# Kernel tuning notes

Measured on AMD Instinct MI355X. Metric: run time of the kernel, lower is better.

The kernel has to match this reference:

```python
import jax, jax.numpy as jnp
import numpy as np
from jax import lax

B, C, H, W = 16, 128, 64, 64
S = 16  # d_state


def setup_inputs() -> dict:
    key = jax.random.key(0)
    ks = jax.random.split(key, 12)
    d = {
        'x': jax.random.normal(ks[0], (B, C, H, W), jnp.float32),
        'conv_w': jax.random.normal(ks[1], (C, C, 3, 3), jnp.float32) * (1.0 / np.sqrt(C * 9)),
        'conv_b': jax.random.normal(ks[2], (C,), jnp.float32) * 0.01,
        'dt_w': jax.random.normal(ks[3], (C, C), jnp.float32) * (1.0 / np.sqrt(C)),
        'dt_b': jax.random.normal(ks[4], (C,), jnp.float32) * 0.01,
        'A': jax.random.normal(ks[5], (C, S), jnp.float32),
        'D': jax.random.normal(ks[6], (C,), jnp.float32),
        'g1_w': jax.random.normal(ks[7], (C, C), jnp.float32) * (1.0 / np.sqrt(C)),
        'g1_b': jax.random.normal(ks[8], (C,), jnp.float32) * 0.01,
        'g2_w': jax.random.normal(ks[9], (C, C), jnp.float32) * (1.0 / np.sqrt(C)),
        'g2_b': jax.random.normal(ks[10], (C,), jnp.float32) * 0.01,
    }
    return d


def _forward(x, conv_w, conv_b, dt_w, dt_b, A, D, g1_w, g1_b, g2_w, g2_b):
    identity = x
    # 3x3 conv, padding=1 (SAME)
    x = lax.conv_general_dilated(x, conv_w, (1, 1), 'SAME',
                                 dimension_numbers=('NCHW', 'OIHW', 'NCHW'))
    x = x + conv_b[None, :, None, None]
    # spectral gate: global avg pool -> 1x1 conv -> relu -> 1x1 conv -> sigmoid
    pooled = jnp.mean(x, axis=(2, 3))                       # [B, C]
    g = jax.nn.relu(jnp.einsum('bc,oc->bo', pooled, g1_w) + g1_b)
    g = jax.nn.sigmoid(jnp.einsum('bc,oc->bo', g, g2_w) + g2_b)
    x = x * g[:, :, None, None]
    # ssm scan over H*W tokens
    x_seq = x.transpose(0, 2, 3, 1).reshape(x.shape[0], H * W, C)  # [B, L, C]
    dt = jax.nn.sigmoid(jnp.einsum('blc,oc->blo', x_seq, dt_w) + dt_b)
    An = -jnp.exp(A)   # [C, S]
    Dp = jnp.exp(D)    # [C]

    def step(h, inp):
        xt, dtt = inp  # each [B, C]
        h = h * jnp.exp(An[None] * dtt[:, :, None]) + xt[:, :, None]  # [B, C, S]
        y = jnp.sum(h * An[None], axis=-1) + Dp * xt                   # [B, C]
        return h, y

    h0 = jnp.zeros((x.shape[0], C, S), x.dtype)
    xs = (x_seq.transpose(1, 0, 2), dt.transpose(1, 0, 2))  # [L, B, C]
    _, ys = lax.scan(step, h0, xs)                           # ys: [L, B, C]
    y = ys.transpose(1, 0, 2).reshape(x.shape[0], H, W, C).transpose(0, 3, 1, 2)
    return y + identity


def reference(x, conv_w, conv_b, dt_w, dt_b, A, D, g1_w, g1_b, g2_w, g2_b):
    return _forward(x, conv_w, conv_b, dt_w, dt_b, A, D, g1_w, g1_b, g2_w, g2_b)
```

## Files before the change

### kernel.cpp

```cpp
#include <hip/hip_runtime.h>
#include <hip/hip_bf16.h>
#include <stdint.h>

#define BB 16
#define CC 128
#define HH 64
#define WW 64
#define LL 4096
#define SS 16
#define NCH 64
#define CT 64

typedef __attribute__((ext_vector_type(2))) float f32x2;
typedef __attribute__((ext_vector_type(4))) float f32x4;
typedef __attribute__((ext_vector_type(8))) short short8;
typedef __attribute__((ext_vector_type(4))) unsigned int u32x4;

#define AS1 __attribute__((address_space(1)))
#define AS3 __attribute__((address_space(3)))

__device__ __forceinline__ float bf2f(unsigned short u) {
    union { unsigned int i; float f; } v;
    v.i = ((unsigned int)u) << 16;
    return v.f;
}
__device__ __forceinline__ float asf(unsigned int u) {
    union { unsigned int i; float f; } v;
    v.i = u;
    return v.f;
}
__device__ __forceinline__ unsigned short f2bf(float f) {
    union { float f; unsigned int i; } v;
    v.f = f;
    unsigned int x = v.i;
    return (unsigned short)((x + 0x7fffu + ((x >> 16) & 1u)) >> 16);
}
__device__ __forceinline__ float fexp2(float x) { return __builtin_amdgcn_exp2f(x); }

__global__ __launch_bounds__(256) void k0(const float* __restrict__ x, unsigned short* __restrict__ xT,
                                          const float* __restrict__ conv_w, const float* __restrict__ dt_w,
                                          const float* __restrict__ A, const float* __restrict__ Dv,
                                          const float* __restrict__ g1w, const float* __restrict__ g2w,
                                          short* __restrict__ wf, short* __restrict__ wdtf,
                                          float* __restrict__ An, float* __restrict__ An2, float* __restrict__ Dp,
                                          float* __restrict__ pooled, float* __restrict__ g1wT, float* __restrict__ g2wT) {
    __shared__ float lt[64][65];
    int bid = blockIdx.x;
    int tid = threadIdx.x;
    if (bid < 2048) {
        int b = bid >> 7, rem = bid & 127;
        int tt = rem >> 1, ct = rem & 1;
        int t0 = tt * 64, c0 = ct * 64;
        int colr = tid & 63, rowb = tid >> 6;
#pragma unroll
        for (int r = 0; r < 16; ++r) {
            int row = rowb + r * 4;
            lt[row][colr] = x[(size_t)(b * CC + c0 + row) * LL + t0 + colr];
        }
        __syncthreads();
#pragma unroll
        for (int r = 0; r < 16; ++r) {
            int trow = rowb + r * 4;
            xT[((size_t)b * LL + t0 + trow) * CC + c0 + colr] = f2bf(lt[colr][trow]);
        }
        return;
    }
    int idx = (bid - 2048) * 256 + tid;
    if (idx < 18432) {
        int lane = idx & 63, fr = idx >> 6;
        int nfg = fr & 7, ks = (fr >> 3) & 3, tp = fr >> 5;
        int dy = tp / 3, dx = tp % 3;
        int cout = nfg * 16 + (lane & 15);
        int cin0 = ks * 32 + (lane >> 4) * 8;
        short8 v;
#pragma unroll
        for (int j = 0; j < 8; ++j)
            v[j] = (short)f2bf(conv_w[((cout * CC + cin0 + j) * 3 + dy) * 3 + dx]);
        *(short8*)(wf + (size_t)idx * 8) = v;
    } else if (idx < 20480) {
        int i2 = idx - 18432;
        int lane = i2 & 63, fr = i2 >> 6;
        int nfg = fr & 7, ks = fr >> 3;
        int o = nfg * 16 + (lane & 15);
        int c0 = ks * 32 + (lane >> 4) * 8;
        short8 v;
#pragma unroll
        for (int j = 0; j < 8; ++j) v[j] = (short)f2bf(dt_w[o * CC + c0 + j]);
        *(short8*)(wdtf + (size_t)i2 * 8) = v;
    } else if (idx < 22528) {
        int i3 = idx - 20480;
        float a = -expf(A[i3]);
        An[i3] = a;
        An2[i3] = a * 1.4426950408889634f;
    } else if (idx < 22656) {
        int c = idx - 22528;
        Dp[c] = expf(Dv[c]);
    } else if (idx < 24704) {
        pooled[idx - 22656] = 0.f;
    } else if (idx < 41088) {
        int i = idx - 24704;
        int c = i >> 7, o = i & 127;
        g1wT[i] = g1w[o * 128 + c];
    } else if (idx < 57472) {
        int i = idx - 41088;
        int c = i >> 7, o = i & 127;
        g2wT[i] = g2w[o * 128 + c];
    }
}

__global__ __launch_bounds__(256) void k1(const unsigned short* __restrict__ xT,
                                          const short* __restrict__ wf,
                                          const float* __restrict__ conv_b,
                                          unsigned short* __restrict__ convT,
                                          float* __restrict__ pooled) {
    __shared__ __align__(16) unsigned short slab[3 * 66 * 128];
    int bid = blockIdx.x;
    int b = bid >> 6, h = bid & 63;
    int tid = threadIdx.x;
    int wave = tid >> 6, lane = tid & 63;

    if (tid < 96) {
        int dy = tid >> 5, r = (tid >> 4) & 1, j = tid & 15;
        u32x4 z = {0, 0, 0, 0};
        *(u32x4*)((char*)slab + dy * 16896 + (r ? 16640 : 0) + j * 16) = z;
    }
#pragma unroll
    for (int dy = 0; dy < 3; ++dy) {
        int hs = h + dy - 1;
        char* slabdy = (char*)slab + dy * 16896;
        if (hs >= 0 && hs < HH) {
            const char* src = (const char*)xT + (size_t)(b * LL + hs * 64) * 256;
#pragma unroll
            for (int i = 0; i < 4; ++i) {
                unsigned int Xbase = 256u + (unsigned)i * 4096u + (unsigned)wave * 1024u;
                unsigned int X = Xbase + (unsigned)lane * 16u;
                unsigned int tok = X >> 8;
                unsigned int srcoff = ((X & ~255u) - 256u) | ((X & 255u) ^ ((tok & 7u) << 4));
                __builtin_amdgcn_global_load_lds((const AS1 unsigned int*)(src + srcoff),
                                                 (AS3 unsigned int*)(slabdy + Xbase), 16, 0, 0);
            }
        } else {
            u32x4 z = {0, 0, 0, 0};
#pragma unroll
            for (int i = 0; i < 4; ++i)
                *(u32x4*)(slabdy + 256 + tid * 64 + i * 16) = z;
        }
    }
    __syncthreads();

    int lm = lane & 15, lg = lane >> 4;
    f32x4 acc[4][2];
#pragma unroll
    for (int m = 0; m < 4; ++m)
#pragma unroll
        for (int n = 0; n < 2; ++n) acc[m][n] = (f32x4){0.f, 0.f, 0.f, 0.f};

#pragma unroll
    for (int tp = 0; tp < 9; ++tp) {
        int dy = tp / 3, dx = tp % 3;
        const char* slabdy = (const char*)slab + dy * 16896;
#pragma unroll
        for (int ks = 0; ks < 4; ++ks) {
            short8 bf0 = *(const short8*)(wf + ((size_t)(((tp * 4 + ks) * 8) + wave * 2 + 0) * 64 + lane) * 8);
            short8 bf1 = *(const short8*)(wf + ((size_t)(((tp * 4 + ks) * 8) + wave * 2 + 1) * 64 + lane) * 8);
#pragma unroll
            for (int mf = 0; mf < 4; ++mf) {
                int tok = mf * 16 + lm + dx;
                unsigned int off = (unsigned)((tok * 256 + ks * 64 + lg * 16) ^ ((tok & 7) << 4));
                short8 af = *(const short8*)(slabdy + off);
                acc[mf][0] = __builtin_amdgcn_mfma_f32_16x16x32_bf16(af, bf0, acc[mf][0], 0, 0, 0);
                acc[mf][1] = __builtin_amdgcn_mfma_f32_16x16x32_bf16(af, bf1, acc[mf][1], 0, 0, 0);
            }
        }
    }

    int n0w = wave * 32;
    size_t tokbase = (size_t)(b * LL + h * 64);
    float psum[2] = {0.f, 0.f};
#pragma unroll
    for (int nf = 0; nf < 2; ++nf) {
        int n = n0w + nf * 16 + lm;
        float bias = conv_b[n];
#pragma unroll
        for (int mf = 0; mf < 4; ++mf)
#pragma unroll
            for (int r = 0; r < 4; ++r) {
                int w = mf * 16 + lg * 4 + r;
                float v = acc[mf][nf][r] + bias;
                convT[(tokbase + w) * CC + n] = f2bf(v);
                psum[nf] += v;
            }
    }
#pragma unroll
    for (int nf = 0; nf < 2; ++nf) {
        float s = psum[nf];
        s += __shfl_xor(s, 16);
        s += __shfl_xor(s, 32);
        if (lane < 16) atomicAdd(&pooled[b * CC + n0w + nf * 16 + lane], s);
    }
}

__global__ __launch_bounds__(128) void k2(const float* __restrict__ pooled,
                                          const float* __restrict__ g1wT, const float* __restrict__ g1b,
                                          const float* __restrict__ g2wT, const float* __restrict__ g2b,
                                          float* __restrict__ gate) {
    __shared__ float meanr[128];
    __shared__ float garr[128];
    int b = blockIdx.x;
    int tid = threadIdx.x;
    meanr[tid] = pooled[b * CC + tid] * (1.f / 4096.f);
    __syncthreads();
    float acc = g1b[tid];
    for (int c = 0; c < 128; ++c) acc += meanr[c] * g1wT[c * 128 + tid];
    garr[tid] = fmaxf(acc, 0.f);
    __syncthreads();
    float acc2 = g2b[tid];
    for (int c = 0; c < 128; ++c) acc2 += garr[c] * g2wT[c * 128 + tid];
    gate[b * CC + tid] = __builtin_amdgcn_rcpf(1.f + fexp2(-1.4426950408889634f * acc2));
}

__global__ __launch_bounds__(256) void k3(const unsigned short* __restrict__ convT,
                                          const short* __restrict__ wdtf,
                                          const float* __restrict__ gate,
                                          const float* __restrict__ dt_b,
                                          const float* __restrict__ An2,
                                          unsigned short* __restrict__ dtT,
                                          unsigned int* __restrict__ xdt,
                                          float* __restrict__ hend, float* __restrict__ decay,
                                          int packed) {
    __shared__ __align__(16) unsigned short albuf[64 * 128];
    __shared__ __align__(16) unsigned short dtl[64 * 136];
    __shared__ float gl[128];
    int bid = blockIdx.x;
    int b = bid >> 6, ch = bid & 63, t0 = ch * 64;
    int tid = threadIdx.x;
    int wave = tid >> 6, lane = tid & 63;

    if (tid < 128) gl[tid] = gate[b * CC + tid];
    __syncthreads();

    const char* srcb = (const char*)convT + (size_t)(b * LL + t0) * 256;
#pragma unroll
    for (int i = 0; i < 4; ++i) {
        unsigned int byteoff = (unsigned)((i * 256 + tid) * 16);
        unsigned int tok = byteoff >> 8;
        unsigned int inner = byteoff & 255u;
        int c8 = (int)(inner >> 1);
        short8 v = *(const short8*)(srcb + (size_t)tok * 256 + inner);
#pragma unroll
        for (int j = 0; j < 8; ++j) {
            float f = bf2f((unsigned short)v[j]) * gl[c8 + j];
            v[j] = (short)f2bf(f);
        }
        *(short8*)((char*)albuf + (byteoff ^ ((tok & 7u) << 4))) = v;
    }
    __syncthreads();

    int lm = lane & 15, lg = lane >> 4;
    f32x4 acc[4][2];
#pragma unroll
    for (int m = 0; m < 4; ++m)
#pragma unroll
        for (int n = 0; n < 2; ++n) acc[m][n] = (f32x4){0.f, 0.f, 0.f, 0.f};
#pragma unroll
    for (int ks = 0; ks < 4; ++ks) {
        short8 bf0 = *(const short8*)(wdtf + ((size_t)((ks * 8) + wave * 2 + 0) * 64 + lane) * 8);
        short8 bf1 = *(const short8*)(wdtf + ((size_t)((ks * 8) + wave * 2 + 1) * 64 + lane) * 8);
#pragma unroll
        for (int mf = 0; mf < 4; ++mf) {
            int tok = mf * 16 + lm;
            unsigned int off = (unsigned)((tok * 256 + ks * 64 + lg * 16) ^ ((tok & 7) << 4));
            short8 af = *(const short8*)((const char*)albuf + off);
            acc[mf][0] = __builtin_amdgcn_mfma_f32_16x16x32_bf16(af, bf0, acc[mf][0], 0, 0, 0);
            acc[mf][1] = __builtin_amdgcn_mfma_f32_16x16x32_bf16(af, bf1, acc[mf][1], 0, 0, 0);
        }
    }
#pragma unroll
    for (int nf = 0; nf < 2; ++nf) {
        int o = wave * 32 + nf * 16 + lm;
        float zb = dt_b[o];
#pragma unroll
        for (int mf = 0; mf < 4; ++mf)
#pragma unroll
            for (int r = 0; r < 4; ++r) {
                int tok = mf * 16 + lg * 4 + r;
                float z = acc[mf][nf][r] + zb;
                float d = __builtin_amdgcn_rcpf(1.f + fexp2(-1.4426950408889634f * z));
                unsigned short ub = f2bf(d);
                if (!packed) dtT[(size_t)(b * LL + t0 + tok) * CC + o] = ub;
                dtl[tok * 136 + o] = ub;
            }
    }
    __syncthreads();

    if (packed) {
        unsigned int* xdblk = xdt + ((size_t)b * LL + t0) * CC;
        int tq = tid >> 5, c0 = (tid & 31) * 4;
#pragma unroll
        for (int k = 0; k < 8; ++k) {
            int t = k * 8 + tq;
            unsigned int xoff = ((unsigned)(t * 256 + c0 * 2)) ^ (((unsigned)t & 7u) << 4);
            const unsigned short* xu4 = (const unsigned short*)((const char*)albuf + xoff);
            const unsigned short* du4 = &dtl[t * 136 + c0];
            u32x4 w4;
#pragma unroll
            for (int j = 0; j < 4; ++j)
                w4[j] = (((unsigned int)du4[j]) << 16) | (unsigned int)xu4[j];
            *(u32x4*)(xdblk + (size_t)t * CC + c0) = w4;
        }
    }

    int c = tid & 127, shalf = tid >> 7, s0 = shalf * 8;
    float a2[8], h[8];
#pragma unroll
    for (int q = 0; q < 2; ++q) {
        f32x4 av = *(const f32x4*)(An2 + c * SS + s0 + q * 4);
#pragma unroll
        for (int j = 0; j < 4; ++j) { a2[q * 4 + j] = av[j]; h[q * 4 + j] = 0.f; }
    }
    float sdt = 0.f;
#pragma unroll 4
    for (int t = 0; t < CT; ++t) {
        unsigned int xoff = ((unsigned)(t * 256 + c * 2)) ^ (((unsigned)t & 7u) << 4);
        float x = bf2f(*(const unsigned short*)((const char*)albuf + xoff));
        float d = bf2f(dtl[t * 136 + c]);
        sdt += d;
#pragma unroll
        for (int s = 0; s < 8; ++s) h[s] = h[s] * fexp2(a2[s] * d) + x;
    }
    size_t base = ((size_t)(b * NCH + ch) * CC + c) * SS + s0;
#pragma unroll
    for (int q = 0; q < 2; ++q) {
        f32x4 hv, dv;
#pragma unroll
        for (int j = 0; j < 4; ++j) {
            hv[j] = h[q * 4 + j];
            dv[j] = fexp2(a2[q * 4 + j] * sdt);
        }
        *(f32x4*)(hend + base + q * 4) = hv;
        *(f32x4*)(decay + base + q * 4) = dv;
    }
}

__global__ __launch_bounds__(256) void k5(const float* __restrict__ hend, const float* __restrict__ decay,
                                          float* __restrict__ H0) {
    int idx = blockIdx.x * 256 + threadIdx.x;
    int b = idx >> 11, rem = idx & 2047;
    float Hv = 0.f;
    for (int k = 0; k < NCH; ++k) {
        size_t base = (size_t)(b * NCH + k) * 2048 + rem;
        H0[base] = Hv;
        Hv = hend[base] + Hv * decay[base];
    }
}

__global__ __launch_bounds__(256, 4) void k6p(const unsigned int* __restrict__ xdt,
                                              const float* __restrict__ Antab,
                                              const float* __restrict__ An2tab,
                                              const float* __restrict__ Dp,
                                              const float* __restrict__ H0,
                                              const float* __restrict__ xin,
                                              float* __restrict__ out) {
    __shared__ unsigned short ylds[128][66];
    int bid = blockIdx.x;
    int b = bid >> 6, ch = bid & 63;
    int tid = threadIdx.x;
    int wave = tid >> 6, lane = tid & 63;
    int t0 = ch * CT;
    int c = wave * 32 + (lane & 31);
    int shalf = lane >> 5;
    int s0 = shalf * 8;

    f32x2 a22[4], anv[4], h2[4];
#pragma unroll
    for (int q = 0; q < 2; ++q) {
        f32x4 av = *(const f32x4*)(An2tab + c * SS + s0 + q * 4);
        f32x4 nv = *(const f32x4*)(Antab + c * SS + s0 + q * 4);
        a22[q * 2 + 0] = (f32x2){av[0], av[1]};
        a22[q * 2 + 1] = (f32x2){av[2], av[3]};
        anv[q * 2 + 0] = (f32x2){nv[0], nv[1]};
        anv[q * 2 + 1] = (f32x2){nv[2], nv[3]};
    }
    size_t hbase = ((size_t)(b * NCH + ch) * CC + c) * SS + s0;
#pragma unroll
    for (int q = 0; q < 2; ++q) {
        f32x4 hv = *(const f32x4*)(H0 + hbase + q * 4);
        h2[q * 2 + 0] = (f32x2){hv[0], hv[1]};
        h2[q * 2 + 1] = (f32x2){hv[2], hv[3]};
    }
    float dpc = (shalf == 0) ? Dp[c] : 0.f;
    const unsigned int* xdp = xdt + ((size_t)b * LL + t0) * CC + c;

#pragma unroll 8
    for (int t = 0; t < CT; ++t) {
        unsigned int w = xdp[(size_t)t * CC];
        float x = asf(w << 16);
        float d = asf(w & 0xffff0000u);
        f32x2 x2 = {x, x};
        f32x2 d2 = {d, d};
        f32x2 y2 = {0.f, 0.f};
#pragma unroll
        for (int q = 0; q < 4; ++q) {
            f32x2 tq = a22[q] * d2;
            f32x2 e2;
            e2.x = fexp2(tq.x);
            e2.y = fexp2(tq.y);
            h2[q] = h2[q] * e2 + x2;
            y2 += h2[q] * anv[q];
        }
        float yp = y2.x + y2.y + dpc * x;
        float yo = yp + __shfl_xor(yp, 32);
        if (shalf == 0) ylds[c][t] = f2bf(yo);
    }
    __syncthreads();

    int tt = tid & 63, wq = tid >> 6;
    size_t outbase = (size_t)b * CC * LL + t0 + tt;
#pragma unroll 4
    for (int rr = 0; rr < 32; ++rr) {
        int row = rr * 4 + wq;
        size_t gi = outbase + (size_t)row * LL;
        out[gi] = bf2f(ylds[row][tt]) + xin[gi];
    }
}

__global__ __launch_bounds__(256, 4) void k6f(const unsigned short* __restrict__ convT,
                                              const unsigned short* __restrict__ dtT,
                                              const float* __restrict__ gate,
                                              const float* __restrict__ Antab,
                                              const float* __restrict__ An2tab,
                                              const float* __restrict__ Dp,
                                              const float* __restrict__ H0,
                                              const float* __restrict__ xin,
                                              float* __restrict__ out) {
    __shared__ unsigned short ylds[128][66];
    int bid = blockIdx.x;
    int b = bid >> 6, ch = bid & 63;
    int tid = threadIdx.x;
    int wave = tid >> 6, lane = tid & 63;
    int t0 = ch * CT;
    int c = wave * 32 + (lane & 31);
    int shalf = lane >> 5;
    int s0 = shalf * 8;

    float a2[8], an[8], h[8];
#pragma unroll
    for (int q = 0; q < 2; ++q) {
        f32x4 av = *(const f32x4*)(An2tab + c * SS + s0 + q * 4);
        f32x4 nv = *(const f32x4*)(Antab + c * SS + s0 + q * 4);
#pragma unroll
        for (int j = 0; j < 4; ++j) { a2[q * 4 + j] = av[j]; an[q * 4 + j] = nv[j]; }
    }
    size_t hbase = ((size_t)(b * NCH + ch) * CC + c) * SS + s0;
#pragma unroll
    for (int q = 0; q < 2; ++q) {
        f32x4 hv = *(const f32x4*)(H0 + hbase + q * 4);
#pragma unroll
        for (int j = 0; j < 4; ++j) h[q * 4 + j] = hv[j];
    }
    float g = gate[b * CC + c];
    float dpc = (shalf == 0) ? Dp[c] : 0.f;
    const unsigned short* xp = convT + (size_t)(b * LL + t0) * CC + c;
    const unsigned short* dp = dtT + (size_t)(b * LL + t0) * CC + c;

#pragma unroll 4
    for (int t = 0; t < CT; ++t) {
        float x = bf2f(xp[t * CC]) * g;
        float d = bf2f(dp[t * CC]);
        float y0 = dpc * x, y1 = 0.f;
#pragma unroll
        for (int s = 0; s < 8; ++s) {
            h[s] = h[s] * fexp2(a2[s] * d) + x;
            if (s & 1) y1 += h[s] * an[s]; else y0 += h[s] * an[s];
        }
        float yp = y0 + y1;
        float yo = yp + __shfl_xor(yp, 32);
        if (shalf == 0) ylds[c][t] = f2bf(yo);
    }
    __syncthreads();

    int tt = tid & 63, wq = tid >> 6;
    size_t outbase = (size_t)b * CC * LL + t0 + tt;
#pragma unroll 4
    for (int rr = 0; rr < 32; ++rr) {
        int row = rr * 4 + wq;
        size_t gi = outbase + (size_t)row * LL;
        out[gi] = bf2f(ylds[row][tt]) + xin[gi];
    }
}

extern "C" void kernel_launch(void* const* d_in, const int* in_sizes, int n_in,
                              void* d_out, int out_size, void* d_ws, size_t ws_size,
                              hipStream_t stream) {
    const float* x      = (const float*)d_in[0];
    const float* conv_w = (const float*)d_in[1];
    const float* conv_b = (const float*)d_in[2];
    const float* dt_w   = (const float*)d_in[3];
    const float* dt_b   = (const float*)d_in[4];
    const float* A      = (const float*)d_in[5];
    const float* D      = (const float*)d_in[6];
    const float* g1w    = (const float*)d_in[7];
    const float* g1b    = (const float*)d_in[8];
    const float* g2w    = (const float*)d_in[9];
    const float* g2b    = (const float*)d_in[10];
    float* outp         = (float*)d_out;
    char* ws = (char*)d_ws;

    const bool P = (ws_size >= 67600896ull);

    unsigned short* xT;
    float *hend, *decay, *H0, *g1wT, *g2wT, *pooled, *gate, *Antab, *An2tab, *Dp;
    unsigned short *convT, *dtT;
    unsigned int* xdt;
    short *wf, *wdtf;

    if (P) {
        xT     = (unsigned short*)(ws + 0);
        hend   = (float*)(ws + 0);
        decay  = (float*)(ws + 8388608);
        convT  = (unsigned short*)(ws + 16777216);
        H0     = (float*)(ws + 16777216);
        xdt    = (unsigned int*)(ws + 33554432);
        dtT    = (unsigned short*)(ws + 33554432);
        wf     = (short*)(ws + 67108864);
        wdtf   = (short*)(ws + 67403776);
        pooled = (float*)(ws + 67436544);
        gate   = (float*)(ws + 67444736);
        Antab  = (float*)(ws + 67452928);
        An2tab = (float*)(ws + 67461120);
        Dp     = (float*)(ws + 67469312);
        g1wT   = (float*)(ws + 67469824);
        g2wT   = (float*)(ws + 67535360);
    } else {
        xT     = (unsigned short*)(ws + 0);
        hend   = (float*)(ws + 0);
        decay  = (float*)(ws + 8388608);
        convT  = (unsigned short*)(ws + 16777216);
        dtT    = (unsigned short*)(ws + 33554432);
        xdt    = (unsigned int*)(ws + 33554432);
        H0     = (float*)(ws + 50331648);
        g1wT   = (float*)(ws + 50331648);
        g2wT   = (float*)(ws + 50397184);
        wf     = (short*)(ws + 58720256);
        wdtf   = (short*)(ws + 59015168);
        pooled = (float*)(ws + 59047936);
        gate   = (float*)(ws + 59056128);
        Antab  = (float*)(ws + 59064320);
        An2tab = (float*)(ws + 59072512);
        Dp     = (float*)(ws + 59080704);
    }

    hipLaunchKernelGGL(k0, dim3(2273), dim3(256), 0, stream, x, xT, conv_w, dt_w, A, D, g1w, g2w,
                       wf, wdtf, Antab, An2tab, Dp, pooled, g1wT, g2wT);
    hipLaunchKernelGGL(k1, dim3(1024), dim3(256), 0, stream, xT, wf, conv_b, convT, pooled);
    hipLaunchKernelGGL(k2, dim3(16), dim3(128), 0, stream, pooled, g1wT, g1b, g2wT, g2b, gate);
    hipLaunchKernelGGL(k3, dim3(1024), dim3(256), 0, stream, convT, wdtf, gate, dt_b, An2tab,
                       dtT, xdt, hend, decay, (int)P);
    hipLaunchKernelGGL(k5, dim3(128), dim3(256), 0, stream, hend, decay, H0);
    if (P) {
        hipLaunchKernelGGL(k6p, dim3(1024), dim3(256), 0, stream, (const unsigned int*)xdt,
                           Antab, An2tab, Dp, H0, x, outp);
    } else {
        hipLaunchKernelGGL(k6f, dim3(1024), dim3(256), 0, stream, convT, dtT, gate,
                           Antab, An2tab, Dp, H0, x, outp);
    }
}
```

Measured before the change: 126.3 us.

## Store packed x/dt buffer channel-major and vectorize scan loads and output epilogue

The packed x/dt intermediate changes from token-major [B,L,C] to channel-major [B,C,L]. Each scan thread can then fetch four consecutive timesteps with one 128-bit load instead of one strided 32-bit load per step. The producer write loop is remapped to gather four tokens per channel from LDS. The final residual-add epilogue also switches to float4 loads and stores. The cost is more scattered LDS reads in the producer, and the layout must stay consistent with any other consumer of the buffer.

```diff
diff --git a/kernel.cpp b/kernel.cpp
--- a/kernel.cpp
+++ b/kernel.cpp
@@ -294,19 +294,21 @@
     __syncthreads();
 
     if (packed) {
-        unsigned int* xdblk = xdt + ((size_t)b * LL + t0) * CC;
-        int tq = tid >> 5, c0 = (tid & 31) * 4;
+        int tquad = tid & 15;
+        int cb = tid >> 4;
 #pragma unroll
         for (int k = 0; k < 8; ++k) {
-            int t = k * 8 + tq;
-            unsigned int xoff = ((unsigned)(t * 256 + c0 * 2)) ^ (((unsigned)t & 7u) << 4);
-            const unsigned short* xu4 = (const unsigned short*)((const char*)albuf + xoff);
-            const unsigned short* du4 = &dtl[t * 136 + c0];
+            int c = k * 16 + cb;
             u32x4 w4;
 #pragma unroll
-            for (int j = 0; j < 4; ++j)
-                w4[j] = (((unsigned int)du4[j]) << 16) | (unsigned int)xu4[j];
-            *(u32x4*)(xdblk + (size_t)t * CC + c0) = w4;
+            for (int j = 0; j < 4; ++j) {
+                int t = tquad * 4 + j;
+                unsigned int xoff = ((unsigned)(t * 256 + c * 2)) ^ (((unsigned)t & 7u) << 4);
+                unsigned short xu = *(const unsigned short*)((const char*)albuf + xoff);
+                unsigned short du = dtl[t * 136 + c];
+                w4[j] = (((unsigned int)du) << 16) | (unsigned int)xu;
+            }
+            *(u32x4*)(xdt + ((size_t)b * CC + c) * LL + t0 + tquad * 4) = w4;
         }
     }
 
@@ -389,38 +391,45 @@
         h2[q * 2 + 1] = (f32x2){hv[2], hv[3]};
     }
     float dpc = (shalf == 0) ? Dp[c] : 0.f;
-    const unsigned int* xdp = xdt + ((size_t)b * LL + t0) * CC + c;
-
-#pragma unroll 8
-    for (int t = 0; t < CT; ++t) {
-        unsigned int w = xdp[(size_t)t * CC];
-        float x = asf(w << 16);
-        float d = asf(w & 0xffff0000u);
-        f32x2 x2 = {x, x};
-        f32x2 d2 = {d, d};
-        f32x2 y2 = {0.f, 0.f};
-#pragma unroll
-        for (int q = 0; q < 4; ++q) {
-            f32x2 tq = a22[q] * d2;
-            f32x2 e2;
-            e2.x = fexp2(tq.x);
-            e2.y = fexp2(tq.y);
-            h2[q] = h2[q] * e2 + x2;
-            y2 += h2[q] * anv[q];
-        }
-        float yp = y2.x + y2.y + dpc * x;
-        float yo = yp + __shfl_xor(yp, 32);
-        if (shalf == 0) ylds[c][t] = f2bf(yo);
-    }
-    __syncthreads();
-
-    int tt = tid & 63, wq = tid >> 6;
-    size_t outbase = (size_t)b * CC * LL + t0 + tt;
+    const u32x4* xdp = (const u32x4*)(xdt + ((size_t)b * CC + c) * LL + t0);
+
 #pragma unroll 4
-    for (int rr = 0; rr < 32; ++rr) {
-        int row = rr * 4 + wq;
-        size_t gi = outbase + (size_t)row * LL;
-        out[gi] = bf2f(ylds[row][tt]) + xin[gi];
+    for (int t4 = 0; t4 < 16; ++t4) {
+        u32x4 w4 = xdp[t4];
+#pragma unroll
+        for (int j = 0; j < 4; ++j) {
+            unsigned int w = w4[j];
+            float x = asf(w << 16);
+            float d = asf(w & 0xffff0000u);
+            f32x2 x2 = {x, x};
+            f32x2 d2 = {d, d};
+            f32x2 y2 = {0.f, 0.f};
+#pragma unroll
+            for (int q = 0; q < 4; ++q) {
+                f32x2 tq = a22[q] * d2;
+                f32x2 e2;
+                e2.x = fexp2(tq.x);
+                e2.y = fexp2(tq.y);
+                h2[q] = h2[q] * e2 + x2;
+                y2 += h2[q] * anv[q];
+            }
+            float yp = y2.x + y2.y + dpc * x;
+            float yo = yp + __shfl_xor(yp, 32);
+            if (shalf == 0) ylds[c][t4 * 4 + j] = f2bf(yo);
+        }
+    }
+    __syncthreads();
+
+    int tq = tid & 15, rbase = tid >> 4;
+#pragma unroll
+    for (int k = 0; k < 8; ++k) {
+        int row = k * 16 + rbase;
+        size_t gi = (size_t)(b * CC + row) * LL + t0 + tq * 4;
+        f32x4 xi = *(const f32x4*)(xin + gi);
+        f32x4 yo;
+#pragma unroll
+        for (int j = 0; j < 4; ++j) yo[j] = bf2f(ylds[row][tq * 4 + j]) + xi[j];
+        *(f32x4*)(out + gi) = yo;
     }
 }
 
```

New measurement: 122.2 us, median of 2. 1.03x faster.
